# Optimization experiments

Measured on AMD Instinct MI355X. Metric: run time of the kernel, lower is better.

## Reference

```python
import jax, jax.numpy as jnp
import numpy as np

EMBED_DIM = 1024
HEADS = 16
HEAD_DIM = EMBED_DIM // HEADS
BATCH = 4
SEQ = 1024


def setup_inputs() -> dict:
    key = jax.random.key(0)
    ks = jax.random.split(key, 9)
    s = 1.0 / np.sqrt(HEAD_DIM)
    so = 1.0 / np.sqrt(EMBED_DIM)
    return {
        "values": jax.random.normal(ks[0], (BATCH, SEQ, EMBED_DIM), dtype=jnp.float32),
        "query": jax.random.normal(ks[1], (BATCH, SEQ, EMBED_DIM), dtype=jnp.float32),
        "key": jax.random.normal(ks[2], (BATCH, SEQ, EMBED_DIM), dtype=jnp.float32),
        "mask": jax.random.randint(ks[3], (BATCH, 1, SEQ, SEQ), 0, 2, dtype=jnp.int32),
        "Wv": jax.random.uniform(ks[4], (HEAD_DIM, HEAD_DIM), jnp.float32, -s, s),
        "Wk": jax.random.uniform(ks[5], (HEAD_DIM, HEAD_DIM), jnp.float32, -s, s),
        "Wq": jax.random.uniform(ks[6], (HEAD_DIM, HEAD_DIM), jnp.float32, -s, s),
        "Wo": jax.random.uniform(ks[7], (EMBED_DIM, EMBED_DIM), jnp.float32, -so, so),
        "bo": jax.random.uniform(ks[8], (EMBED_DIM,), jnp.float32, -so, so),
    }


def reference(values, query, key, mask, Wv, Wk, Wq, Wo, bo):
    N, Lq, E = query.shape
    Lk = key.shape[1]
    H, D = HEADS, HEAD_DIM
    # reshape to heads, then per-head shared linear projection (Linear(head_dim, head_dim), no bias)
    v = jnp.einsum('nlhd,ed->nlhe', values.reshape(N, Lk, H, D), Wv)
    k = jnp.einsum('nlhd,ed->nlhe', key.reshape(N, Lk, H, D), Wk)
    q = jnp.einsum('nlhd,ed->nlhe', query.reshape(N, Lq, H, D), Wq)
    # full [N,H,Q,K] scores, scaled by 1/sqrt(embed_dim) as in source
    sim = jnp.einsum('nqhd,nkhd->nhqk', q, k)
    sim = jnp.where(mask == 0, jnp.float32(-1e20), sim)
    attn = jax.nn.softmax(sim / jnp.sqrt(jnp.float32(E)), axis=3)
    out = jnp.einsum('nhqk,nkhd->nqhd', attn, v).reshape(N, Lq, H * D)
    return out @ Wo.T + bo
```

## Files before the change

### kernel.cpp

```cpp
#include <hip/hip_runtime.h>

#define SEQ 1024
#define HEADS 16
#define HD 64
#define EMB 1024

typedef short bf16x8 __attribute__((ext_vector_type(8)));
typedef float f32x4 __attribute__((ext_vector_type(4)));

static __device__ __forceinline__ unsigned short f2bf(float f) {
  unsigned u = __builtin_bit_cast(unsigned, f);
  u += 0x7FFFu + ((u >> 16) & 1u);
  return (unsigned short)(u >> 16);
}

static __device__ __forceinline__ unsigned cvtpk(float a, float b) {
  unsigned r;
  asm("v_cvt_pk_bf16_f32 %0, %1, %2" : "=v"(r) : "v"(a), "v"(b));
  return r;
}

static __device__ __forceinline__ void gload_lds16(const void* g, void* l) {
  __builtin_amdgcn_global_load_lds((const __attribute__((address_space(1))) unsigned int*)g,
                                   (__attribute__((address_space(3))) unsigned int*)l,
                                   16, 0, 0);
}

__global__ __launch_bounds__(256) void k_maskpack(const int* __restrict__ mask,
                                                  unsigned long long* __restrict__ mb) {
  const unsigned gw = (blockIdx.x * 256u + threadIdx.x) >> 6;
  const unsigned lane = threadIdx.x & 63u;
  const int v = mask[(size_t)gw * 64u + lane];
  const unsigned long long bits = __ballot(v != 0);
  if (lane == 0) {
    const unsigned n = gw >> 14, qrow = (gw >> 4) & 1023u, ktile = gw & 15u;
    mb[((size_t)n * 16 + ktile) * 1024 + qrow] = bits;
  }
}

__global__ __launch_bounds__(256) void k_cvtwo(const float* __restrict__ Wo,
                                               const float* __restrict__ Wv,
                                               const float* __restrict__ Wq,
                                               const float* __restrict__ Wk,
                                               unsigned short* __restrict__ wob,
                                               unsigned short* __restrict__ wb) {
  const unsigned tid = threadIdx.x;
  if (blockIdx.x < 1024) {
    const unsigned gid = blockIdx.x * 256u + tid;
    const unsigned e = gid >> 8, rem = gid & 255u;
    const unsigned blk = rem >> 4, cc = rem & 15u;
    const float* src = Wo + (size_t)e * 1024 + blk * 64 + cc;
    const unsigned w0 = cvtpk(src[0], src[16]);
    const unsigned w1 = cvtpk(src[32], src[48]);
    *(uint2*)(wob + (size_t)gid * 4) = make_uint2(w0, w1);
  } else {
    #pragma unroll
    for (int t = 0; t < 3; ++t) {
      const float* src = (t == 0) ? Wv : (t == 1) ? Wq : Wk;
      const float sc = (t == 1) ? 0.045084220027786356f : 1.0f;
      const float4 f0 = *(const float4*)(src + tid * 16);
      const float4 f1 = *(const float4*)(src + tid * 16 + 4);
      const float4 f2 = *(const float4*)(src + tid * 16 + 8);
      const float4 f3 = *(const float4*)(src + tid * 16 + 12);
      uint4 u0, u1;
      u0.x = cvtpk(f0.x * sc, f0.y * sc); u0.y = cvtpk(f0.z * sc, f0.w * sc);
      u0.z = cvtpk(f1.x * sc, f1.y * sc); u0.w = cvtpk(f1.z * sc, f1.w * sc);
      u1.x = cvtpk(f2.x * sc, f2.y * sc); u1.y = cvtpk(f2.z * sc, f2.w * sc);
      u1.z = cvtpk(f3.x * sc, f3.y * sc); u1.w = cvtpk(f3.z * sc, f3.w * sc);
      *(uint4*)(wb + t * 4096 + tid * 16) = u0;
      *(uint4*)(wb + t * 4096 + tid * 16 + 8) = u1;
    }
  }
}

__global__ __launch_bounds__(256) void k_proj(const float* __restrict__ values,
                                              const float* __restrict__ query,
                                              const float* __restrict__ key,
                                              const unsigned short* __restrict__ wb,
                                              unsigned short* __restrict__ vb,
                                              unsigned short* __restrict__ qb,
                                              unsigned short* __restrict__ kb) {
  const int lane = threadIdx.x & 63;
  const int c = lane & 15, g = lane >> 4;
  const int wid = blockIdx.x * 4 + (threadIdx.x >> 6);
  const int t = wid >> 12;
  const int rem = wid & 4095;
  const int n = rem >> 10;
  const int h = (rem >> 6) & 15;
  const int lb = rem & 63;

  const float* x; unsigned short* out;
  if (t == 0)      { x = values; out = vb; }
  else if (t == 1) { x = query;  out = qb; }
  else             { x = key;    out = kb; }
  const unsigned short* W = wb + t * 4096;

  bf16x8 a[2];
  const float* xr = x + ((size_t)n * SEQ + lb * 16 + c) * EMB + h * HD;
  #pragma unroll
  for (int ks = 0; ks < 2; ++ks) {
    const float4 f0 = *(const float4*)(xr + ks * 32 + g * 8);
    const float4 f1 = *(const float4*)(xr + ks * 32 + g * 8 + 4);
    uint4 u;
    u.x = cvtpk(f0.x, f0.y); u.y = cvtpk(f0.z, f0.w);
    u.z = cvtpk(f1.x, f1.y); u.w = cvtpk(f1.z, f1.w);
    a[ks] = __builtin_bit_cast(bf16x8, u);
  }

  f32x4 acc[4] = {};
  #pragma unroll
  for (int cb = 0; cb < 4; ++cb) {
    #pragma unroll
    for (int ks = 0; ks < 2; ++ks) {
      const bf16x8 b = *(const bf16x8*)(W + (cb * 16 + c) * HD + ks * 32 + g * 8);
      acc[cb] = __builtin_amdgcn_mfma_f32_16x16x32_bf16(a[ks], b, acc[cb], 0, 0, 0);
    }
  }

  if (t == 0) {
    unsigned short* vt = out + (size_t)(n * HEADS + h) * (HD * SEQ);
    const int key0 = lb * 16 + 4 * g;
    #pragma unroll
    for (int cb = 0; cb < 4; ++cb) {
      const unsigned w0 = cvtpk(acc[cb][0], acc[cb][1]);
      const unsigned w1 = cvtpk(acc[cb][2], acc[cb][3]);
      *(uint2*)(vt + (size_t)(cb * 16 + c) * SEQ + key0) = make_uint2(w0, w1);
    }
  } else {
    unsigned short* op = out + ((size_t)(n * HEADS + h) * SEQ + lb * 16) * HD;
    #pragma unroll
    for (int r = 0; r < 4; ++r) {
      const unsigned w0 = cvtpk(acc[0][r], acc[1][r]);
      const unsigned w1 = cvtpk(acc[2][r], acc[3][r]);
      *(uint2*)(op + (4 * g + r) * HD + 4 * c) = make_uint2(w0, w1);
    }
  }
}

__global__ __launch_bounds__(256, 4) void k_attn(const unsigned short* __restrict__ qb,
                                                 const unsigned short* __restrict__ kb,
                                                 const unsigned short* __restrict__ vb,
                                                 const unsigned long long* __restrict__ mb,
                                                 unsigned short* __restrict__ ob) {
  const int tid = threadIdx.x;
  const int w = tid >> 6, lane = tid & 63;
  const int c = lane & 15, g = lane >> 4;
  const int bid = blockIdx.x;
  const int nh = bid & 63, q64 = bid >> 6;
  const int n = nh >> 4, h = nh & 15;
  const int qlo = q64 * 64 + w * 16;

  __shared__ unsigned short Ks[2][64][64];
  __shared__ unsigned short Vs[2][64][64];

  char* const Kb0 = (char*)&Ks[0][0][0];
  char* const Vb0 = (char*)&Vs[0][0][0];

  const size_t nhb = (size_t)(n * HEADS + h) * (SEQ * HD);
  const unsigned short* qp = qb + nhb;
  const char* kpB = (const char*)(kb + nhb);
  const char* vpB = (const char*)(vb + nhb);

  bf16x8 qa[2];
  #pragma unroll
  for (int ks = 0; ks < 2; ++ks)
    qa[ks] = *(const bf16x8*)(qp + (size_t)(qlo + c) * HD + ks * 32 + g * 8);

  bf16x8 ones;
  #pragma unroll
  for (int j = 0; j < 8; ++j) ones[j] = (short)0x3F80;

  f32x4 o[4] = {};
  f32x4 lacc = {};

#define STAGEKV(dstK, dstV, kt_) do {                                                   \
    _Pragma("unroll")                                                                   \
    for (int i = 0; i < 2; ++i) {                                                       \
      const int off = i * 4096 + tid * 16;                                              \
      const int row = off >> 7, slot = (off >> 4) & 7;                                  \
      const int krow = ((row >> 4) & 1) * 32 + ((row >> 5) & 1) * 4 +                   \
                       ((row >> 2) & 3) * 8 + (row & 3);                                \
      const int sw = (slot ^ (row & 7)) << 4;                                           \
      gload_lds16(kpB + (size_t)(kt_) * 8192 + krow * 128 + sw, (dstK) + off);          \
      gload_lds16(vpB + (size_t)row * 2048 + (kt_) * 128 + sw, (dstV) + off);           \
    }                                                                                   \
  } while (0)

  STAGEKV(Kb0, Vb0, 0);
  __syncthreads();

  for (int kt = 0; kt < 16; ++kt) {
    const int cur = kt & 1;
    char* const Kc = Kb0 + cur * 8192;
    char* const Vc = Vb0 + cur * 8192;
    if (kt < 15) STAGEKV(Kb0 + (cur ^ 1) * 8192, Vb0 + (cur ^ 1) * 8192, kt + 1);

    const unsigned long long bits = mb[((size_t)(n * 16 + kt)) * 1024 + qlo + c];
    const unsigned blo = (unsigned)bits, bhi = (unsigned)(bits >> 32);

    bf16x8 kf[4][2];
    #pragma unroll
    for (int sub = 0; sub < 4; ++sub) {
      const int rho = sub * 16 + c;
      #pragma unroll
      for (int ks = 0; ks < 2; ++ks)
        kf[sub][ks] = *(const bf16x8*)(Kc + rho * 128 + (((ks * 4 + g) ^ (c & 7)) << 4));
    }

    bf16x8 vf[4][2];
    #pragma unroll
    for (int db = 0; db < 4; ++db) {
      const int row = db * 16 + c;
      #pragma unroll
      for (int ks = 0; ks < 2; ++ks)
        vf[db][ks] = *(const bf16x8*)(Vc + row * 128 + (((ks * 4 + g) ^ (c & 7)) << 4));
    }

    f32x4 s[4];
    __builtin_amdgcn_s_setprio(1);
    #pragma unroll
    for (int sub = 0; sub < 4; ++sub) {
      f32x4 acc = {};
      acc = __builtin_amdgcn_mfma_f32_16x16x32_bf16(kf[sub][0], qa[0], acc, 0, 0, 0);
      acc = __builtin_amdgcn_mfma_f32_16x16x32_bf16(kf[sub][1], qa[1], acc, 0, 0, 0);
      s[sub] = acc;
    }
    __builtin_amdgcn_s_setprio(0);

    unsigned pw[2][4];
    #pragma unroll
    for (int sub = 0; sub < 4; ++sub) {
      const unsigned x = ((sub & 1) ? bhi : blo) >> (8 * g + ((sub >> 1) << 2));
      const float p0 = (x & 1u) ? __builtin_exp2f(s[sub][0]) : 0.f;
      const float p1 = (x & 2u) ? __builtin_exp2f(s[sub][1]) : 0.f;
      const float p2 = (x & 4u) ? __builtin_exp2f(s[sub][2]) : 0.f;
      const float p3 = (x & 8u) ? __builtin_exp2f(s[sub][3]) : 0.f;
      pw[sub & 1][(sub >> 1) * 2 + 0] = cvtpk(p0, p1);
      pw[sub & 1][(sub >> 1) * 2 + 1] = cvtpk(p2, p3);
    }
    bf16x8 pa[2];
    pa[0] = __builtin_bit_cast(bf16x8, *(uint4*)&pw[0][0]);
    pa[1] = __builtin_bit_cast(bf16x8, *(uint4*)&pw[1][0]);

    __builtin_amdgcn_s_setprio(1);
    #pragma unroll
    for (int ks = 0; ks < 2; ++ks) {
      #pragma unroll
      for (int db = 0; db < 4; ++db)
        o[db] = __builtin_amdgcn_mfma_f32_16x16x32_bf16(pa[ks], vf[db][ks], o[db], 0, 0, 0);
      lacc = __builtin_amdgcn_mfma_f32_16x16x32_bf16(pa[ks], ones, lacc, 0, 0, 0);
    }
    __builtin_amdgcn_s_setprio(0);

    __syncthreads();
  }
#undef STAGEKV

  #pragma unroll
  for (int r = 0; r < 4; ++r) {
    const float inv = 1.0f / lacc[r];
    const unsigned w0 = cvtpk(o[0][r] * inv, o[1][r] * inv);
    const unsigned w1 = cvtpk(o[2][r] * inv, o[3][r] * inv);
    *(uint2*)(ob + ((size_t)n * SEQ + qlo + 4 * g + r) * EMB + h * 64 + 4 * c) =
        make_uint2(w0, w1);
  }
}

__global__ __launch_bounds__(256, 4) void k_gemm(const unsigned short* __restrict__ A,
                                                 const unsigned short* __restrict__ B,
                                                 const float* __restrict__ bo,
                                                 float* __restrict__ C) {
  const int tid = threadIdx.x;
  const int w = tid >> 6, lane = tid & 63;
  const int c = lane & 15, g = lane >> 4;
  const int bm = blockIdx.x & 63, bn = blockIdx.x >> 6;
  const int m0 = bm * 64, n0 = bn * 64;
  const int wr = w >> 1, wc = w & 1;

  __shared__ unsigned short As[2][64][64];
  __shared__ unsigned short Bs[2][64][64];

  f32x4 acc[2][2] = {};

#define STAGE(buf, kt_) do {                                                             \
    _Pragma("unroll")                                                                    \
    for (int i = 0; i < 2; ++i) {                                                        \
      const int off = i * 4096 + tid * 16;                                               \
      const int row = off >> 7, slot = (off >> 4) & 7;                                   \
      const int sw = (slot ^ (row & 7)) << 4;                                            \
      gload_lds16((const char*)A + ((size_t)(m0 + row) * 1024 + (kt_) * 64) * 2 + sw,    \
                  (char*)&As[buf][0][0] + off);                                          \
      gload_lds16((const char*)B + ((size_t)(n0 + row) * 1024 + (kt_) * 64) * 2 + sw,    \
                  (char*)&Bs[buf][0][0] + off);                                          \
    }                                                                                    \
  } while (0)

  STAGE(0, 0);
  __syncthreads();

  for (int kt = 0; kt < 16; ++kt) {
    const int cur = kt & 1;
    if (kt < 15) STAGE(cur ^ 1, kt + 1);
    #pragma unroll
    for (int ks = 0; ks < 2; ++ks) {
      bf16x8 af[2], bf_[2];
      #pragma unroll
      for (int i = 0; i < 2; ++i) {
        const int row = wr * 32 + i * 16 + c;
        af[i] = *(const bf16x8*)((char*)&As[cur][0][0] + row * 128 +
                                 (((ks * 4 + g) ^ (c & 7)) << 4));
      }
      #pragma unroll
      for (int j = 0; j < 2; ++j) {
        const int row = wc * 32 + j * 16 + c;
        bf_[j] = *(const bf16x8*)((char*)&Bs[cur][0][0] + row * 128 +
                                  (((ks * 4 + g) ^ (c & 7)) << 4));
      }
      __builtin_amdgcn_s_setprio(1);
      #pragma unroll
      for (int i = 0; i < 2; ++i)
        #pragma unroll
        for (int j = 0; j < 2; ++j)
          acc[i][j] = __builtin_amdgcn_mfma_f32_16x16x32_bf16(af[i], bf_[j], acc[i][j], 0, 0, 0);
      __builtin_amdgcn_s_setprio(0);
    }
    __syncthreads();
  }
#undef STAGE

  #pragma unroll
  for (int j = 0; j < 2; ++j) {
    const int col = n0 + wc * 32 + j * 16 + c;
    const float bv = bo[col];
    #pragma unroll
    for (int i = 0; i < 2; ++i) {
      const int rowb = m0 + wr * 32 + i * 16 + 4 * g;
      #pragma unroll
      for (int r = 0; r < 4; ++r)
        C[(size_t)(rowb + r) * 1024 + col] = acc[i][j][r] + bv;
    }
  }
}

extern "C" void kernel_launch(void* const* d_in, const int* in_sizes, int n_in,
                              void* d_out, int out_size, void* d_ws, size_t ws_size,
                              hipStream_t stream) {
  const float* values = (const float*)d_in[0];
  const float* query  = (const float*)d_in[1];
  const float* key    = (const float*)d_in[2];
  const int*   mask   = (const int*)d_in[3];
  const float* Wv     = (const float*)d_in[4];
  const float* Wk     = (const float*)d_in[5];
  const float* Wq     = (const float*)d_in[6];
  const float* Wo     = (const float*)d_in[7];
  const float* bo     = (const float*)d_in[8];
  float* out = (float*)d_out;

  char* ws = (char*)d_ws;
  unsigned short* qb = (unsigned short*)(ws);
  unsigned short* kb = (unsigned short*)(ws + (size_t)8 * 1024 * 1024);
  unsigned short* vb = (unsigned short*)(ws + (size_t)16 * 1024 * 1024);
  unsigned short* ob = (unsigned short*)(ws + (size_t)24 * 1024 * 1024);
  unsigned long long* mb = (unsigned long long*)(ws + (size_t)32 * 1024 * 1024);
  unsigned short* wb  = (unsigned short*)(ws + (size_t)32 * 1024 * 1024 + 512 * 1024);
  unsigned short* wob = (unsigned short*)(ws + (size_t)33 * 1024 * 1024);

  k_maskpack<<<16384, 256, 0, stream>>>(mask, mb);
  k_cvtwo<<<1025, 256, 0, stream>>>(Wo, Wv, Wq, Wk, wob, wb);
  k_proj<<<3072, 256, 0, stream>>>(values, query, key, wb, vb, qb, kb);
  k_attn<<<1024, 256, 0, stream>>>(qb, kb, vb, mb, ob);
  k_gemm<<<1024, 256, 0, stream>>>(ob, wob, bo, out);
}
```

Baseline: 86.31 us.

## Merge prep kernels and use partial vmcnt waits for double-buffered staging

Merges the mask-packing and weight-conversion kernels into a single launch, removing one kernel boundary. In the attention and output GEMM kernels, it hoists the per-thread staging address math out of the loop. It replaces full __syncthreads with a partial s_waitcnt vmcnt(4) plus raw s_barrier, so the next tile's loads stay in flight while the current tile is consumed. It also moves the V fragment LDS reads after the QK MFMAs to overlap them. The hand-written waitcnt relies on the compiler not reordering or inserting other vector-memory ops, which is a correctness risk. The mask bits load inside the loop also counts toward vmcnt.

```diff
diff --git a/kernel.cpp b/kernel.cpp
--- a/kernel.cpp
+++ b/kernel.cpp
@@ -26,27 +26,26 @@
                                    16, 0, 0);
 }
 
-__global__ __launch_bounds__(256) void k_maskpack(const int* __restrict__ mask,
-                                                  unsigned long long* __restrict__ mb) {
-  const unsigned gw = (blockIdx.x * 256u + threadIdx.x) >> 6;
-  const unsigned lane = threadIdx.x & 63u;
-  const int v = mask[(size_t)gw * 64u + lane];
-  const unsigned long long bits = __ballot(v != 0);
-  if (lane == 0) {
-    const unsigned n = gw >> 14, qrow = (gw >> 4) & 1023u, ktile = gw & 15u;
-    mb[((size_t)n * 16 + ktile) * 1024 + qrow] = bits;
-  }
-}
-
-__global__ __launch_bounds__(256) void k_cvtwo(const float* __restrict__ Wo,
-                                               const float* __restrict__ Wv,
-                                               const float* __restrict__ Wq,
-                                               const float* __restrict__ Wk,
-                                               unsigned short* __restrict__ wob,
-                                               unsigned short* __restrict__ wb) {
+__global__ __launch_bounds__(256) void k_prep(const int* __restrict__ mask,
+                                              const float* __restrict__ Wo,
+                                              const float* __restrict__ Wv,
+                                              const float* __restrict__ Wq,
+                                              const float* __restrict__ Wk,
+                                              unsigned long long* __restrict__ mb,
+                                              unsigned short* __restrict__ wob,
+                                              unsigned short* __restrict__ wb) {
   const unsigned tid = threadIdx.x;
-  if (blockIdx.x < 1024) {
-    const unsigned gid = blockIdx.x * 256u + tid;
+  if (blockIdx.x < 16384) {
+    const unsigned gw = blockIdx.x * 4u + (tid >> 6);
+    const unsigned lane = tid & 63u;
+    const int v = mask[(size_t)gw * 64u + lane];
+    const unsigned long long bits = __ballot(v != 0);
+    if (lane == 0) {
+      const unsigned n = gw >> 14, qrow = (gw >> 4) & 1023u, ktile = gw & 15u;
+      mb[((size_t)n * 16 + ktile) * 1024 + qrow] = bits;
+    }
+  } else if (blockIdx.x < 17408) {
+    const unsigned gid = (blockIdx.x - 16384) * 256u + tid;
     const unsigned e = gid >> 8, rem = gid & 255u;
     const unsigned blk = rem >> 4, cc = rem & 15u;
     const float* src = Wo + (size_t)e * 1024 + blk * 64 + cc;
@@ -143,12 +142,12 @@
                                                  const unsigned long long* __restrict__ mb,
                                                  unsigned short* __restrict__ ob) {
   const int tid = threadIdx.x;
-  const int w = tid >> 6, lane = tid & 63;
+  const int lane = tid & 63;
   const int c = lane & 15, g = lane >> 4;
   const int bid = blockIdx.x;
   const int nh = bid & 63, q64 = bid >> 6;
   const int n = nh >> 4, h = nh & 15;
-  const int qlo = q64 * 64 + w * 16;
+  const int qlo = q64 * 64 + (tid >> 6) * 16;
 
   __shared__ unsigned short Ks[2][64][64];
   __shared__ unsigned short Vs[2][64][64];
@@ -161,6 +160,19 @@
   const char* kpB = (const char*)(kb + nhb);
   const char* vpB = (const char*)(vb + nhb);
 
+  const char* kSrc[2]; const char* vSrc[2]; int ldsOff[2];
+  #pragma unroll
+  for (int i = 0; i < 2; ++i) {
+    const int off = i * 4096 + tid * 16;
+    const int row = off >> 7, slot = (off >> 4) & 7;
+    const int krow = ((row >> 4) & 1) * 32 + ((row >> 5) & 1) * 4 +
+                     ((row >> 2) & 3) * 8 + (row & 3);
+    const int sw = (slot ^ (row & 7)) << 4;
+    kSrc[i] = kpB + krow * 128 + sw;
+    vSrc[i] = vpB + (size_t)row * 2048 + sw;
+    ldsOff[i] = off;
+  }
+
   bf16x8 qa[2];
   #pragma unroll
   for (int ks = 0; ks < 2; ++ks)
@@ -173,27 +185,27 @@
   f32x4 o[4] = {};
   f32x4 lacc = {};
 
-#define STAGEKV(dstK, dstV, kt_) do {                                                   \
-    _Pragma("unroll")                                                                   \
-    for (int i = 0; i < 2; ++i) {                                                       \
-      const int off = i * 4096 + tid * 16;                                              \
-      const int row = off >> 7, slot = (off >> 4) & 7;                                  \
-      const int krow = ((row >> 4) & 1) * 32 + ((row >> 5) & 1) * 4 +                   \
-                       ((row >> 2) & 3) * 8 + (row & 3);                                \
-      const int sw = (slot ^ (row & 7)) << 4;                                           \
-      gload_lds16(kpB + (size_t)(kt_) * 8192 + krow * 128 + sw, (dstK) + off);          \
-      gload_lds16(vpB + (size_t)row * 2048 + (kt_) * 128 + sw, (dstV) + off);           \
-    }                                                                                   \
+#define STAGEKV(dstK, dstV, kt_) do {                                   \
+    _Pragma("unroll")                                                   \
+    for (int i = 0; i < 2; ++i) {                                       \
+      gload_lds16(kSrc[i] + (size_t)(kt_) * 8192, (dstK) + ldsOff[i]);  \
+      gload_lds16(vSrc[i] + (kt_) * 128, (dstV) + ldsOff[i]);           \
+    }                                                                   \
   } while (0)
 
   STAGEKV(Kb0, Vb0, 0);
-  __syncthreads();
 
   for (int kt = 0; kt < 16; ++kt) {
     const int cur = kt & 1;
     char* const Kc = Kb0 + cur * 8192;
     char* const Vc = Vb0 + cur * 8192;
-    if (kt < 15) STAGEKV(Kb0 + (cur ^ 1) * 8192, Vb0 + (cur ^ 1) * 8192, kt + 1);
+    if (kt < 15) {
+      STAGEKV(Kb0 + (cur ^ 1) * 8192, Vb0 + (cur ^ 1) * 8192, kt + 1);
+      asm volatile("s_waitcnt vmcnt(4)" ::: "memory");
+    } else {
+      asm volatile("s_waitcnt vmcnt(0)" ::: "memory");
+    }
+    asm volatile("s_barrier" ::: "memory");
 
     const unsigned long long bits = mb[((size_t)(n * 16 + kt)) * 1024 + qlo + c];
     const unsigned blo = (unsigned)bits, bhi = (unsigned)(bits >> 32);
@@ -205,15 +217,6 @@
       #pragma unroll
       for (int ks = 0; ks < 2; ++ks)
         kf[sub][ks] = *(const bf16x8*)(Kc + rho * 128 + (((ks * 4 + g) ^ (c & 7)) << 4));
-    }
-
-    bf16x8 vf[4][2];
-    #pragma unroll
-    for (int db = 0; db < 4; ++db) {
-      const int row = db * 16 + c;
-      #pragma unroll
-      for (int ks = 0; ks < 2; ++ks)
-        vf[db][ks] = *(const bf16x8*)(Vc + row * 128 + (((ks * 4 + g) ^ (c & 7)) << 4));
     }
 
     f32x4 s[4];
@@ -226,6 +229,15 @@
       s[sub] = acc;
     }
     __builtin_amdgcn_s_setprio(0);
+
+    bf16x8 vf[4][2];
+    #pragma unroll
+    for (int db = 0; db < 4; ++db) {
+      const int row = db * 16 + c;
+      #pragma unroll
+      for (int ks = 0; ks < 2; ++ks)
+        vf[db][ks] = *(const bf16x8*)(Vc + row * 128 + (((ks * 4 + g) ^ (c & 7)) << 4));
+    }
 
     unsigned pw[2][4];
     #pragma unroll
@@ -252,7 +264,7 @@
     }
     __builtin_amdgcn_s_setprio(0);
 
-    __syncthreads();
+    if (kt < 15) asm volatile("s_barrier" ::: "memory");
   }
 #undef STAGEKV
 
@@ -280,27 +292,39 @@
   __shared__ unsigned short As[2][64][64];
   __shared__ unsigned short Bs[2][64][64];
 
+  const char* aSrc[2]; const char* bSrc[2]; int ldsOff[2];
+  #pragma unroll
+  for (int i = 0; i < 2; ++i) {
+    const int off = i * 4096 + tid * 16;
+    const int row = off >> 7, slot = (off >> 4) & 7;
+    const int sw = (slot ^ (row & 7)) << 4;
+    aSrc[i] = (const char*)A + (size_t)(m0 + row) * 2048 + sw;
+    bSrc[i] = (const char*)B + (size_t)(n0 + row) * 2048 + sw;
+    ldsOff[i] = off;
+  }
+
   f32x4 acc[2][2] = {};
 
-#define STAGE(buf, kt_) do {                                                             \
-    _Pragma("unroll")                                                                    \
-    for (int i = 0; i < 2; ++i) {                                                        \
-      const int off = i * 4096 + tid * 16;                                               \
-      const int row = off >> 7, slot = (off >> 4) & 7;                                   \
-      const int sw = (slot ^ (row & 7)) << 4;                                            \
-      gload_lds16((const char*)A + ((size_t)(m0 + row) * 1024 + (kt_) * 64) * 2 + sw,    \
-                  (char*)&As[buf][0][0] + off);                                          \
-      gload_lds16((const char*)B + ((size_t)(n0 + row) * 1024 + (kt_) * 64) * 2 + sw,    \
-                  (char*)&Bs[buf][0][0] + off);                                          \
-    }                                                                                    \
+#define STAGE(buf, kt_) do {                                                  \
+    _Pragma("unroll")                                                         \
+    for (int i = 0; i < 2; ++i) {                                             \
+      gload_lds16(aSrc[i] + (kt_) * 128, (char*)&As[buf][0][0] + ldsOff[i]);  \
+      gload_lds16(bSrc[i] + (kt_) * 128, (char*)&Bs[buf][0][0] + ldsOff[i]);  \
+    }                                                                         \
   } while (0)
 
   STAGE(0, 0);
-  __syncthreads();
 
   for (int kt = 0; kt < 16; ++kt) {
     const int cur = kt & 1;
-    if (kt < 15) STAGE(cur ^ 1, kt + 1);
+    if (kt < 15) {
+      STAGE(cur ^ 1, kt + 1);
+      asm volatile("s_waitcnt vmcnt(4)" ::: "memory");
+    } else {
+      asm volatile("s_waitcnt vmcnt(0)" ::: "memory");
+    }
+    asm volatile("s_barrier" ::: "memory");
+
     #pragma unroll
     for (int ks = 0; ks < 2; ++ks) {
       bf16x8 af[2], bf_[2];
@@ -324,7 +348,8 @@
           acc[i][j] = __builtin_amdgcn_mfma_f32_16x16x32_bf16(af[i], bf_[j], acc[i][j], 0, 0, 0);
       __builtin_amdgcn_s_setprio(0);
     }
-    __syncthreads();
+
+    if (kt < 15) asm volatile("s_barrier" ::: "memory");
   }
 #undef STAGE
 
@@ -365,8 +390,7 @@
   unsigned short* wb  = (unsigned short*)(ws + (size_t)32 * 1024 * 1024 + 512 * 1024);
   unsigned short* wob = (unsigned short*)(ws + (size_t)33 * 1024 * 1024);
 
-  k_maskpack<<<16384, 256, 0, stream>>>(mask, mb);
-  k_cvtwo<<<1025, 256, 0, stream>>>(Wo, Wv, Wq, Wk, wob, wb);
+  k_prep<<<17409, 256, 0, stream>>>(mask, Wo, Wv, Wq, Wk, mb, wob, wb);
   k_proj<<<3072, 256, 0, stream>>>(values, query, key, wb, vb, qb, kb);
   k_attn<<<1024, 256, 0, stream>>>(qb, kb, vb, mb, ob);
   k_gemm<<<1024, 256, 0, stream>>>(ob, wob, bo, out);
```

Result: no change. 87.40 us (+1.3%).
